# Kernel optimization log

Hardware: AMD Instinct MI355X
Metric: run time of the kernel (lower is better)

## Reference

```python
import jax, jax.numpy as jnp
import numpy as np

T = 2.0          # temperature (hardcoded to 2 in the torch module)
EPSILON = 0.1    # sinkhorn entropic regularization
N_ITERS = 10     # sinkhorn_loss default n_iters
CLIP_MAX = 10.0  # torch.clamp(Wxy, max=10.0)
EPS = 1e-8
LOSS_SCALE = 0.001


def setup_inputs() -> dict:
    key = jax.random.key(0)
    k1, k2 = jax.random.split(key)
    B, N, D = 4, 256, 512
    y_s = jax.random.normal(k1, (B, N, D), dtype=jnp.float32)
    y_t = jax.random.normal(k2, (B, N, D), dtype=jnp.float32)
    return {"y_s": y_s, "y_t": y_t}


def _sinkhorn_sample(x, y):
    # x, y: [N, D] probability rows. L1 cost matrix [N, N].
    W = jnp.sum(jnp.abs(x[:, None, :] - y[None, :, :]), axis=-1)
    Wc = jnp.minimum(W, CLIP_MAX)
    K = jnp.exp(-Wc / EPSILON) + EPS  # x = x + 1e-8 before normalization

    def step(P, _):
        P = P / jnp.maximum(jnp.sum(P, axis=1, keepdims=True), EPS)
        P = P / jnp.maximum(jnp.sum(P, axis=0, keepdims=True), EPS)
        return P, None

    P, _ = jax.lax.scan(step, K, None, length=N_ITERS)
    return jnp.sum(P * W)


def reference(y_s, y_t):
    p_s = jax.nn.softmax(y_s / T, axis=-1)
    p_t = jax.nn.softmax(y_t / T, axis=-1)
    losses = jax.vmap(_sinkhorn_sample)(p_s, p_t)  # [B]
    # emd_loss = sum_i 0.001 * loss_i; returned value = emd_loss / B
    return LOSS_SCALE * jnp.mean(losses)
```

## Files before the change

kernel.cpp:

```cpp
#include <hip/hip_runtime.h>

#define NB 4
#define NN 256
#define ND 512
#define NITER 10

typedef _Float16 half_t;
typedef __attribute__((ext_vector_type(8))) unsigned short ushort8v;
typedef __attribute__((ext_vector_type(8))) _Float16 half8v;
typedef __attribute__((ext_vector_type(2))) _Float16 half2v;

__device__ __forceinline__ unsigned short f2bf(float x) {
  unsigned u = __float_as_uint(x);
  u += 0x7fffu + ((u >> 16) & 1u);
  return (unsigned short)(u >> 16);
}
__device__ __forceinline__ float bf2f(unsigned short h) {
  return __uint_as_float(((unsigned)h) << 16);
}

__global__ __launch_bounds__(256) void softmax_k(const float* __restrict__ ys,
                                                 const float* __restrict__ yt,
                                                 half_t* __restrict__ ps,
                                                 half_t* __restrict__ pt,
                                                 float* __restrict__ out) {
  int bb = blockIdx.x;
  if (bb == 0 && threadIdx.x == 0) out[0] = 0.0f;
  const float* src = (bb < NB * NN) ? ys : yt;
  half_t* dst      = (bb < NB * NN) ? ps : pt;
  int row = bb & (NB * NN - 1);
  const float* rp = src + (size_t)row * ND;
  half_t* wp = dst + (size_t)row * ND;
  int t = threadIdx.x;
  float a = rp[t];
  float b = rp[t + 256];
  float m = fmaxf(a, b);
  #pragma unroll
  for (int s = 1; s < 64; s <<= 1) m = fmaxf(m, __shfl_xor(m, s));
  __shared__ float red[4];
  int wid = t >> 6;
  if ((t & 63) == 0) red[wid] = m;
  __syncthreads();
  m = fmaxf(fmaxf(red[0], red[1]), fmaxf(red[2], red[3]));
  float e0 = expf((a - m) * 0.5f);
  float e1 = expf((b - m) * 0.5f);
  float ssum = e0 + e1;
  #pragma unroll
  for (int s = 1; s < 64; s <<= 1) ssum += __shfl_xor(ssum, s);
  __syncthreads();
  if ((t & 63) == 0) red[wid] = ssum;
  __syncthreads();
  ssum = red[0] + red[1] + red[2] + red[3];
  float inv = 1.0f / ssum;
  wp[t]       = (half_t)(e0 * inv);
  wp[t + 256] = (half_t)(e1 * inv);
}

__global__ __launch_bounds__(256) void cost_k(const half_t* __restrict__ ps,
                                              const half_t* __restrict__ pt,
                                              half_t* __restrict__ W) {
  __shared__ half_t xs[32 * 512];
  __shared__ half_t ysh[32 * 512];
  int b  = blockIdx.z;
  int It = blockIdx.y * 32;
  int Jt = blockIdx.x * 32;
  int t = threadIdx.x;
  const half8v* xg = reinterpret_cast<const half8v*>(ps + ((size_t)b * NN + It) * ND);
  const half8v* yg = reinterpret_cast<const half8v*>(pt + ((size_t)b * NN + Jt) * ND);
  half8v* xsv = reinterpret_cast<half8v*>(xs);
  half8v* ysv = reinterpret_cast<half8v*>(ysh);
  #pragma unroll
  for (int s = 0; s < 8; ++s) {
    int qidx = s * 256 + t;
    int r = qidx >> 6;
    int q = qidx & 63;
    int rot = (r + (r >> 3)) & 7;
    int dst = r * 64 + ((q + rot) & 63);
    xsv[dst] = xg[qidx];
    ysv[dst] = yg[qidx];
  }
  __syncthreads();
  int tx = t & 15, ty = t >> 4;
  int i0 = 2 * ty, j0 = 2 * tx;
  int rx0 = (i0 + (i0 >> 3)) & 7;
  int rx1 = ((i0 + 1) + ((i0 + 1) >> 3)) & 7;
  int ry0 = (j0 + (j0 >> 3)) & 7;
  int ry1 = ((j0 + 1) + ((j0 + 1) >> 3)) & 7;
  float a00 = 0.f, a01 = 0.f, a10 = 0.f, a11 = 0.f;
  #pragma unroll 4
  for (int qq = 0; qq < 64; ++qq) {
    half8v x0 = xsv[i0 * 64 + ((qq + rx0) & 63)];
    half8v x1 = xsv[(i0 + 1) * 64 + ((qq + rx1) & 63)];
    half8v y0 = ysv[j0 * 64 + ((qq + ry0) & 63)];
    half8v y1 = ysv[(j0 + 1) * 64 + ((qq + ry1) & 63)];
    #pragma unroll
    for (int e = 0; e < 8; ++e) {
      float xf0 = (float)x0[e], xf1 = (float)x1[e];
      float yf0 = (float)y0[e], yf1 = (float)y1[e];
      a00 += fabsf(xf0 - yf0);
      a01 += fabsf(xf0 - yf1);
      a10 += fabsf(xf1 - yf0);
      a11 += fabsf(xf1 - yf1);
    }
  }
  half_t* wb = W + ((size_t)b * NN + It + i0) * NN + Jt + j0;
  half2v w0; w0[0] = (half_t)a00; w0[1] = (half_t)a01;
  half2v w1; w1[0] = (half_t)a10; w1[1] = (half_t)a11;
  *reinterpret_cast<half2v*>(wb)      = w0;
  *reinterpret_cast<half2v*>(wb + NN) = w1;
}

__global__ __launch_bounds__(1024) void sink_k(const half_t* __restrict__ Wg,
                                               float* __restrict__ out) {
  __shared__ __align__(16) unsigned short Kl[NN * NN];
  __shared__ __align__(16) float u[NN];
  __shared__ __align__(16) float v[NN];
  __shared__ __align__(16) unsigned short usb[NN];
  __shared__ __align__(16) unsigned short vsb[NN];
  __shared__ __align__(16) float scr[16 * NN];
  int b = blockIdx.x;
  int t = threadIdx.x;
  const half8v* W8 = reinterpret_cast<const half8v*>(Wg + (size_t)b * NN * NN);

  #pragma unroll
  for (int s = 0; s < 8; ++s) {
    int q8 = s * 1024 + t;
    int e = q8 * 8;
    int i = e >> 8;
    int j = e & 255;
    half8v w8 = W8[q8];
    ushort8v kk;
    #pragma unroll
    for (int r = 0; r < 8; ++r) {
      float kf = __expf(fminf((float)w8[r], 10.0f) * -10.0f) + 1e-8f;
      kk[r] = f2bf(kf);
    }
    *reinterpret_cast<ushort8v*>(&Kl[i * 256 + (j ^ ((i & 7) << 3))]) = kk;
  }
  if (t < NN) {
    u[t] = 1.0f; v[t] = 1.0f;
    usb[t] = 0x3F80u; vsb[t] = 0x3F80u;
  }
  __syncthreads();

  for (int it = 0; it < NITER; ++it) {
    {
      int i = t & 255, c = t >> 8;
      const int rowb = i * 256;
      const int sw = (i & 7) << 3;
      float acc = 0.0f;
      #pragma unroll
      for (int q = 0; q < 8; ++q) {
        int j0 = c * 64 + q * 8;
        ushort8v v8 = *reinterpret_cast<const ushort8v*>(&vsb[j0]);
        ushort8v k8 = *reinterpret_cast<const ushort8v*>(&Kl[rowb + (j0 ^ sw)]);
        acc += bf2f(k8[0]) * bf2f(v8[0]) + bf2f(k8[1]) * bf2f(v8[1]) +
               bf2f(k8[2]) * bf2f(v8[2]) + bf2f(k8[3]) * bf2f(v8[3]) +
               bf2f(k8[4]) * bf2f(v8[4]) + bf2f(k8[5]) * bf2f(v8[5]) +
               bf2f(k8[6]) * bf2f(v8[6]) + bf2f(k8[7]) * bf2f(v8[7]);
      }
      scr[c * 256 + i] = acc;
    }
    __syncthreads();
    if (t < NN) {
      float r = scr[t] + scr[256 + t] + scr[512 + t] + scr[768 + t];
      float uo = u[t];
      float un = uo / fmaxf(uo * r, 1e-8f);
      u[t] = un;
      usb[t] = f2bf(un);
    }
    __syncthreads();
    {
      int j4 = t & 63, c = t >> 6;
      int jc = 4 * j4;
      ushort8v ua = *reinterpret_cast<const ushort8v*>(&usb[c * 16]);
      ushort8v uc = *reinterpret_cast<const ushort8v*>(&usb[c * 16 + 8]);
      float acc0 = 0.f, acc1 = 0.f, acc2 = 0.f, acc3 = 0.f;
      #pragma unroll
      for (int q4 = 0; q4 < 4; ++q4) {
        #pragma unroll
        for (int r = 0; r < 4; ++r) {
          int idx = q4 * 4 + r;
          int i = c * 16 + idx;
          float uf = bf2f(idx < 8 ? ua[idx] : uc[idx - 8]);
          ushort4 k4 = *reinterpret_cast<const ushort4*>(&Kl[i * 256 + (jc ^ ((i & 7) << 3))]);
          acc0 += bf2f(k4.x) * uf; acc1 += bf2f(k4.y) * uf;
          acc2 += bf2f(k4.z) * uf; acc3 += bf2f(k4.w) * uf;
        }
      }
      *reinterpret_cast<float4*>(&scr[c * 256 + jc]) = make_float4(acc0, acc1, acc2, acc3);
    }
    __syncthreads();
    if (t < NN) {
      float s0 = 0.0f;
      #pragma unroll
      for (int c = 0; c < 16; ++c) s0 += scr[c * 256 + t];
      float vo = v[t];
      float vn = vo / fmaxf(vo * s0, 1e-8f);
      v[t] = vn;
      vsb[t] = f2bf(vn);
    }
    __syncthreads();
  }

  float acc = 0.0f;
  #pragma unroll
  for (int s = 0; s < 8; ++s) {
    int q8 = s * 1024 + t;
    int e = q8 * 8;
    int i = e >> 8;
    int j = e & 255;
    half8v w8 = W8[q8];
    ushort8v k8 = *reinterpret_cast<const ushort8v*>(&Kl[i * 256 + (j ^ ((i & 7) << 3))]);
    float ui = u[i];
    float4 v0 = *reinterpret_cast<const float4*>(&v[j]);
    float4 v1 = *reinterpret_cast<const float4*>(&v[j + 4]);
    acc += ui * (bf2f(k8[0]) * v0.x * (float)w8[0] + bf2f(k8[1]) * v0.y * (float)w8[1] +
                 bf2f(k8[2]) * v0.z * (float)w8[2] + bf2f(k8[3]) * v0.w * (float)w8[3] +
                 bf2f(k8[4]) * v1.x * (float)w8[4] + bf2f(k8[5]) * v1.y * (float)w8[5] +
                 bf2f(k8[6]) * v1.z * (float)w8[6] + bf2f(k8[7]) * v1.w * (float)w8[7]);
  }
  #pragma unroll
  for (int s = 1; s < 64; s <<= 1) acc += __shfl_xor(acc, s);
  __syncthreads();
  if ((t & 63) == 0) scr[t >> 6] = acc;
  __syncthreads();
  if (t == 0) {
    float tot = 0.0f;
    #pragma unroll
    for (int w = 0; w < 16; ++w) tot += scr[w];
    atomicAdd(out, 2.5e-4f * tot);
  }
}

extern "C" void kernel_launch(void* const* d_in, const int* in_sizes, int n_in,
                              void* d_out, int out_size, void* d_ws, size_t ws_size,
                              hipStream_t stream) {
  const float* ys = (const float*)d_in[0];
  const float* yt = (const float*)d_in[1];
  half_t* ps = (half_t*)d_ws;
  half_t* pt = ps + (size_t)NB * NN * ND;
  half_t* W  = pt + (size_t)NB * NN * ND;
  float* out = (float*)d_out;

  softmax_k<<<2 * NB * NN, 256, 0, stream>>>(ys, yt, ps, pt, out);
  cost_k<<<dim3(8, 8, NB), 256, 0, stream>>>(ps, pt, W);
  sink_k<<<NB, 1024, 0, stream>>>(W, out);
}
```

Before: 108.9 us.

## Move kernel exp into cost kernel and cut Sinkhorn barriers with register scalings

The cost kernel now also computes the bf16 Gibbs kernel K and writes it to global memory, so the single-block-per-batch Sinkhorn kernel only copies K into shared memory instead of doing the exp there. The Sinkhorn loop is restructured so each thread keeps its u and v scalings in registers. Partial row and column sums are reduced with wave shuffles instead of a shared scratch array, which removes two of the four barriers per iteration. This adds an extra global buffer and a K write/read, plus XOR-swizzled u/v layouts to avoid LDS bank conflicts.

Measured after the change: 113.1 us. 1.04x slower.

```diff
diff --git a/kernel.cpp b/kernel.cpp
--- a/kernel.cpp
+++ b/kernel.cpp
@@ -58,7 +58,8 @@
 
 __global__ __launch_bounds__(256) void cost_k(const half_t* __restrict__ ps,
                                               const half_t* __restrict__ pt,
-                                              half_t* __restrict__ W) {
+                                              half_t* __restrict__ W,
+                                              unsigned short* __restrict__ Kg) {
   __shared__ half_t xs[32 * 512];
   __shared__ half_t ysh[32 * 512];
   int b  = blockIdx.z;
@@ -103,118 +104,129 @@
       a11 += fabsf(xf1 - yf1);
     }
   }
-  half_t* wb = W + ((size_t)b * NN + It + i0) * NN + Jt + j0;
+  size_t base = ((size_t)b * NN + It + i0) * NN + Jt + j0;
+  half_t* wb = W + base;
   half2v w0; w0[0] = (half_t)a00; w0[1] = (half_t)a01;
   half2v w1; w1[0] = (half_t)a10; w1[1] = (half_t)a11;
   *reinterpret_cast<half2v*>(wb)      = w0;
   *reinterpret_cast<half2v*>(wb + NN) = w1;
-}
-
-__global__ __launch_bounds__(1024) void sink_k(const half_t* __restrict__ Wg,
+  ushort2 k0, k1;
+  k0.x = f2bf(__expf(fminf(a00, 10.0f) * -10.0f) + 1e-8f);
+  k0.y = f2bf(__expf(fminf(a01, 10.0f) * -10.0f) + 1e-8f);
+  k1.x = f2bf(__expf(fminf(a10, 10.0f) * -10.0f) + 1e-8f);
+  k1.y = f2bf(__expf(fminf(a11, 10.0f) * -10.0f) + 1e-8f);
+  *reinterpret_cast<ushort2*>(Kg + base)      = k0;
+  *reinterpret_cast<ushort2*>(Kg + base + NN) = k1;
+}
+
+__global__ __launch_bounds__(1024) void sink_k(const unsigned short* __restrict__ Kgl,
+                                               const half_t* __restrict__ Wg,
                                                float* __restrict__ out) {
   __shared__ __align__(16) unsigned short Kl[NN * NN];
-  __shared__ __align__(16) float u[NN];
-  __shared__ __align__(16) float v[NN];
-  __shared__ __align__(16) unsigned short usb[NN];
+  __shared__ __align__(16) unsigned short usbT[NN];
   __shared__ __align__(16) unsigned short vsb[NN];
-  __shared__ __align__(16) float scr[16 * NN];
+  __shared__ __align__(16) float u_l[NN];
+  __shared__ __align__(16) float v_l[NN];
+  __shared__ float red[16];
   int b = blockIdx.x;
   int t = threadIdx.x;
-  const half8v* W8 = reinterpret_cast<const half8v*>(Wg + (size_t)b * NN * NN);
-
+  int w = t >> 6, l = t & 63;
+  int l16 = l & 15, grp = l >> 4;
+
+  const ushort8v* Kg8 = reinterpret_cast<const ushort8v*>(Kgl + (size_t)b * NN * NN);
   #pragma unroll
   for (int s = 0; s < 8; ++s) {
     int q8 = s * 1024 + t;
-    int e = q8 * 8;
-    int i = e >> 8;
-    int j = e & 255;
-    half8v w8 = W8[q8];
-    ushort8v kk;
-    #pragma unroll
-    for (int r = 0; r < 8; ++r) {
-      float kf = __expf(fminf((float)w8[r], 10.0f) * -10.0f) + 1e-8f;
-      kk[r] = f2bf(kf);
-    }
+    int i = q8 >> 5;
+    int j = (q8 & 31) * 8;
+    ushort8v kk = Kg8[q8];
     *reinterpret_cast<ushort8v*>(&Kl[i * 256 + (j ^ ((i & 7) << 3))]) = kk;
   }
-  if (t < NN) {
-    u[t] = 1.0f; v[t] = 1.0f;
-    usb[t] = 0x3F80u; vsb[t] = 0x3F80u;
-  }
-  __syncthreads();
+  if (t < NN) { usbT[t] = 0x3F80u; vsb[t] = 0x3F80u; }
+  __syncthreads();
+
+  int irow = w * 16 + l16;
+  const int swr = (irow & 7) << 3;
+  float uo = 1.0f;
+  int jc = w * 16 + 4 * (l & 3);
+  int rch = l >> 2;
+  float vo0 = 1.f, vo1 = 1.f, vo2 = 1.f, vo3 = 1.f;
 
   for (int it = 0; it < NITER; ++it) {
-    {
-      int i = t & 255, c = t >> 8;
-      const int rowb = i * 256;
-      const int sw = (i & 7) << 3;
-      float acc = 0.0f;
-      #pragma unroll
-      for (int q = 0; q < 8; ++q) {
-        int j0 = c * 64 + q * 8;
-        ushort8v v8 = *reinterpret_cast<const ushort8v*>(&vsb[j0]);
-        ushort8v k8 = *reinterpret_cast<const ushort8v*>(&Kl[rowb + (j0 ^ sw)]);
-        acc += bf2f(k8[0]) * bf2f(v8[0]) + bf2f(k8[1]) * bf2f(v8[1]) +
-               bf2f(k8[2]) * bf2f(v8[2]) + bf2f(k8[3]) * bf2f(v8[3]) +
-               bf2f(k8[4]) * bf2f(v8[4]) + bf2f(k8[5]) * bf2f(v8[5]) +
-               bf2f(k8[6]) * bf2f(v8[6]) + bf2f(k8[7]) * bf2f(v8[7]);
-      }
-      scr[c * 256 + i] = acc;
+    float r = 0.0f;
+    #pragma unroll
+    for (int q = 0; q < 8; ++q) {
+      int vpos = (8 * grp + q) ^ grp;
+      ushort8v v8 = *reinterpret_cast<const ushort8v*>(&vsb[vpos * 8]);
+      int j0 = 64 * grp + 8 * q;
+      ushort8v k8 = *reinterpret_cast<const ushort8v*>(&Kl[irow * 256 + (j0 ^ swr)]);
+      r += bf2f(k8[0]) * bf2f(v8[0]) + bf2f(k8[1]) * bf2f(v8[1]) +
+           bf2f(k8[2]) * bf2f(v8[2]) + bf2f(k8[3]) * bf2f(v8[3]) +
+           bf2f(k8[4]) * bf2f(v8[4]) + bf2f(k8[5]) * bf2f(v8[5]) +
+           bf2f(k8[6]) * bf2f(v8[6]) + bf2f(k8[7]) * bf2f(v8[7]);
+    }
+    r += __shfl_xor(r, 16);
+    r += __shfl_xor(r, 32);
+    uo = uo / fmaxf(uo * r, 1e-8f);
+    if (grp == 0) {
+      int tau = l16 * 16 + w;
+      int qd = tau >> 3;
+      usbT[(qd ^ (qd >> 3)) * 8 + (tau & 7)] = f2bf(uo);
     }
     __syncthreads();
-    if (t < NN) {
-      float r = scr[t] + scr[256 + t] + scr[512 + t] + scr[768 + t];
-      float uo = u[t];
-      float un = uo / fmaxf(uo * r, 1e-8f);
-      u[t] = un;
-      usb[t] = f2bf(un);
+
+    int qd2 = 2 * rch;
+    int sq = rch >> 2;
+    int slot_a = qd2 ^ sq;
+    int slot_b = (qd2 + 1) ^ sq;
+    ushort8v u8a = *reinterpret_cast<const ushort8v*>(&usbT[slot_a * 8]);
+    ushort8v u8b = *reinterpret_cast<const ushort8v*>(&usbT[slot_b * 8]);
+    float c0 = 0.f, c1 = 0.f, c2 = 0.f, c3 = 0.f;
+    #pragma unroll
+    for (int rr = 0; rr < 16; ++rr) {
+      int i = rch + 16 * rr;
+      ushort4 k4 = *reinterpret_cast<const ushort4*>(&Kl[i * 256 + (jc ^ ((i & 7) << 3))]);
+      float uf = bf2f(rr < 8 ? u8a[rr] : u8b[rr - 8]);
+      c0 += bf2f(k4.x) * uf; c1 += bf2f(k4.y) * uf;
+      c2 += bf2f(k4.z) * uf; c3 += bf2f(k4.w) * uf;
+    }
+    #pragma unroll
+    for (int m = 4; m <= 32; m <<= 1) {
+      c0 += __shfl_xor(c0, m); c1 += __shfl_xor(c1, m);
+      c2 += __shfl_xor(c2, m); c3 += __shfl_xor(c3, m);
+    }
+    vo0 = vo0 / fmaxf(vo0 * c0, 1e-8f);
+    vo1 = vo1 / fmaxf(vo1 * c1, 1e-8f);
+    vo2 = vo2 / fmaxf(vo2 * c2, 1e-8f);
+    vo3 = vo3 / fmaxf(vo3 * c3, 1e-8f);
+    if (rch == 0) {
+      int qd_v = jc >> 3;
+      int vpos2 = (qd_v ^ (qd_v >> 3)) * 8 + (jc & 7);
+      ushort4 vv;
+      vv.x = f2bf(vo0); vv.y = f2bf(vo1); vv.z = f2bf(vo2); vv.w = f2bf(vo3);
+      *reinterpret_cast<ushort4*>(&vsb[vpos2]) = vv;
     }
     __syncthreads();
-    {
-      int j4 = t & 63, c = t >> 6;
-      int jc = 4 * j4;
-      ushort8v ua = *reinterpret_cast<const ushort8v*>(&usb[c * 16]);
-      ushort8v uc = *reinterpret_cast<const ushort8v*>(&usb[c * 16 + 8]);
-      float acc0 = 0.f, acc1 = 0.f, acc2 = 0.f, acc3 = 0.f;
-      #pragma unroll
-      for (int q4 = 0; q4 < 4; ++q4) {
-        #pragma unroll
-        for (int r = 0; r < 4; ++r) {
-          int idx = q4 * 4 + r;
-          int i = c * 16 + idx;
-          float uf = bf2f(idx < 8 ? ua[idx] : uc[idx - 8]);
-          ushort4 k4 = *reinterpret_cast<const ushort4*>(&Kl[i * 256 + (jc ^ ((i & 7) << 3))]);
-          acc0 += bf2f(k4.x) * uf; acc1 += bf2f(k4.y) * uf;
-          acc2 += bf2f(k4.z) * uf; acc3 += bf2f(k4.w) * uf;
-        }
-      }
-      *reinterpret_cast<float4*>(&scr[c * 256 + jc]) = make_float4(acc0, acc1, acc2, acc3);
-    }
-    __syncthreads();
-    if (t < NN) {
-      float s0 = 0.0f;
-      #pragma unroll
-      for (int c = 0; c < 16; ++c) s0 += scr[c * 256 + t];
-      float vo = v[t];
-      float vn = vo / fmaxf(vo * s0, 1e-8f);
-      v[t] = vn;
-      vsb[t] = f2bf(vn);
-    }
-    __syncthreads();
-  }
-
+  }
+
+  if (grp == 0) u_l[irow] = uo;
+  if (rch == 0) {
+    v_l[jc] = vo0; v_l[jc + 1] = vo1; v_l[jc + 2] = vo2; v_l[jc + 3] = vo3;
+  }
+  __syncthreads();
+
+  const half8v* W8 = reinterpret_cast<const half8v*>(Wg + (size_t)b * NN * NN);
   float acc = 0.0f;
   #pragma unroll
   for (int s = 0; s < 8; ++s) {
     int q8 = s * 1024 + t;
-    int e = q8 * 8;
-    int i = e >> 8;
-    int j = e & 255;
+    int i = q8 >> 5;
+    int j = (q8 & 31) * 8;
     half8v w8 = W8[q8];
     ushort8v k8 = *reinterpret_cast<const ushort8v*>(&Kl[i * 256 + (j ^ ((i & 7) << 3))]);
-    float ui = u[i];
-    float4 v0 = *reinterpret_cast<const float4*>(&v[j]);
-    float4 v1 = *reinterpret_cast<const float4*>(&v[j + 4]);
+    float ui = u_l[i];
+    float4 v0 = *reinterpret_cast<const float4*>(&v_l[j]);
+    float4 v1 = *reinterpret_cast<const float4*>(&v_l[j + 4]);
     acc += ui * (bf2f(k8[0]) * v0.x * (float)w8[0] + bf2f(k8[1]) * v0.y * (float)w8[1] +
                  bf2f(k8[2]) * v0.z * (float)w8[2] + bf2f(k8[3]) * v0.w * (float)w8[3] +
                  bf2f(k8[4]) * v1.x * (float)w8[4] + bf2f(k8[5]) * v1.y * (float)w8[5] +
@@ -223,12 +235,12 @@
   #pragma unroll
   for (int s = 1; s < 64; s <<= 1) acc += __shfl_xor(acc, s);
   __syncthreads();
-  if ((t & 63) == 0) scr[t >> 6] = acc;
+  if (l == 0) red[w] = acc;
   __syncthreads();
   if (t == 0) {
     float tot = 0.0f;
     #pragma unroll
-    for (int w = 0; w < 16; ++w) tot += scr[w];
+    for (int q = 0; q < 16; ++q) tot += red[q];
     atomicAdd(out, 2.5e-4f * tot);
   }
 }
@@ -241,9 +253,10 @@
   half_t* ps = (half_t*)d_ws;
   half_t* pt = ps + (size_t)NB * NN * ND;
   half_t* W  = pt + (size_t)NB * NN * ND;
+  unsigned short* Kg = (unsigned short*)(W + (size_t)NB * NN * NN);
   float* out = (float*)d_out;
 
   softmax_k<<<2 * NB * NN, 256, 0, stream>>>(ys, yt, ps, pt, out);
-  cost_k<<<dim3(8, 8, NB), 256, 0, stream>>>(ps, pt, W);
-  sink_k<<<NB, 1024, 0, stream>>>(W, out);
-}
+  cost_k<<<dim3(8, 8, NB), 256, 0, stream>>>(ps, pt, W, Kg);
+  sink_k<<<NB, 1024, 0, stream>>>(Kg, W, out);
+}
```
